# Kernel optimization log

Measured on AMD Instinct MI355X. Metric: run time of the kernel, lower is better.

The kernel has to match this reference:

```python
import math
import jax, jax.numpy as jnp
import numpy as np

B, L, HID = 2, 2048, 2048
H = 16
D = HID // H  # 128
EPS = 1e-6
ROPE_BASE = 10000.0
BETA_MIN, BETA_MAX = 0.8, 0.9995


def _rope_cache(seq_len, dim):
    half = dim // 2
    inv_freq = 1.0 / (ROPE_BASE ** (jnp.arange(half, dtype=jnp.float32) / float(half)))
    t = jnp.arange(seq_len, dtype=jnp.float32)
    freqs = t[:, None] * inv_freq[None, :]  # [L, half]
    return jnp.cos(freqs), jnp.sin(freqs)


def _apply_rope(x, cos, sin):
    # x: [B, H, L, D]; cos/sin: [L, D//2]
    half = x.shape[-1] // 2
    xe, xo = x[..., :half], x[..., half:]
    c = cos[None, None]
    s = sin[None, None]
    return jnp.concatenate([xe * c - xo * s, xe * s + xo * c], axis=-1)


def setup_inputs() -> dict:
    key = jax.random.key(0)
    ks = jax.random.split(key, 6)
    sc = 1.0 / math.sqrt(HID)  # ~ xavier scale
    return {
        "x": jax.random.normal(ks[0], (B, L, HID), jnp.float32),
        "Wq": jax.random.normal(ks[1], (HID, HID), jnp.float32) * sc,
        "Wk": jax.random.normal(ks[2], (HID, HID), jnp.float32) * sc,
        "Wv": jax.random.normal(ks[3], (HID, HID), jnp.float32) * sc,
        "Wg": jax.random.normal(ks[4], (HID, H), jnp.float32) * sc,
        "bg": jnp.full((H,), math.log(0.98 / (1.0 - 0.98)), jnp.float32),
        "Wo": jax.random.normal(ks[5], (HID, HID), jnp.float32) * sc,
        "bo": jnp.zeros((HID,), jnp.float32),
    }


def _deltanet(x, Wq, Wk, Wv, Wg, bg, Wo, bo):
    Bb, Ll, _ = x.shape
    split = lambda t: t.reshape(Bb, Ll, H, D).transpose(0, 2, 1, 3)  # [B,H,L,D]
    q = split(x @ Wq)
    k = split(x @ Wk)
    v = split(x @ Wv)

    cos, sin = _rope_cache(Ll, D)
    q = _apply_rope(q, cos, sin)
    k = _apply_rope(k, cos, sin)

    beta = jax.nn.sigmoid(x @ Wg + bg)                # [B,L,H]
    beta = jnp.clip(beta, BETA_MIN, BETA_MAX).transpose(0, 2, 1)  # [B,H,L]

    phi_q = jax.nn.elu(q) + 1.0
    phi_k = jax.nn.elu(k) + 1.0

    # time-major for scan
    pq = phi_q.transpose(2, 0, 1, 3)  # [L,B,H,D]
    pk = phi_k.transpose(2, 0, 1, 3)
    vt = v.transpose(2, 0, 1, 3)
    bt = beta.transpose(2, 0, 1)      # [L,B,H]

    S0 = jnp.zeros((Bb, H, D, D), jnp.float32)
    z0 = jnp.zeros((Bb, H, D), jnp.float32)

    def step(carry, inp):
        S, z = carry
        pq_t, pk_t, v_t, b_t = inp
        S = S * b_t[..., None, None] + pk_t[..., :, None] * v_t[..., None, :]
        z = z * b_t[..., None] + pk_t
        numer = jnp.einsum('bhd,bhde->bhe', pq_t, S)
        denom = jnp.sum(pq_t * z, axis=-1, keepdims=True) + EPS
        return (S, z), numer / denom

    (_, _), y = jax.lax.scan(step, (S0, z0), (pq, pk, vt, bt))  # y: [L,B,H,D]
    y = y.transpose(1, 0, 2, 3).reshape(Bb, Ll, HID)  # [B,L,H*D]
    return y @ Wo + bo


def reference(x, Wq, Wk, Wv, Wg, bg, Wo, bo):
    return _deltanet(x, Wq, Wk, Wv, Wg, bg, Wo, bo)
```

## Files before the change

kernel.cpp:

```cpp
#include <hip/hip_runtime.h>


typedef __attribute__((ext_vector_type(8))) short short8;
typedef __attribute__((ext_vector_type(4))) float f32x4;

__device__ __forceinline__ unsigned short f2bf(float f) {
  unsigned u = __float_as_uint(f);
  u += 0x7fffu + ((u >> 16) & 1u);
  return (unsigned short)(u >> 16);
}
__device__ __forceinline__ float bf2f(unsigned short s) {
  return __uint_as_float(((unsigned)s) << 16);
}
__device__ __forceinline__ float phi_elu1(float x) {
  return x > 0.f ? x + 1.f : expf(x);
}
__device__ __forceinline__ void gl_lds16(const void* g, void* l) {
  __builtin_amdgcn_global_load_lds(
      (const __attribute__((address_space(1))) void*)g,
      (__attribute__((address_space(3))) void*)l, 16, 0, 0);
}
__device__ __forceinline__ void bar_raw() {
  asm volatile("" ::: "memory");
  __builtin_amdgcn_s_barrier();
  asm volatile("" ::: "memory");
}

__global__ __launch_bounds__(256)
void k_cast(const float* __restrict__ x, unsigned short* __restrict__ xb) {
  int i = (blockIdx.x * 256 + threadIdx.x) * 4;
  float4 f = *(const float4*)(x + i);
  uint2 p;
  p.x = (unsigned)f2bf(f.x) | ((unsigned)f2bf(f.y) << 16);
  p.y = (unsigned)f2bf(f.z) | ((unsigned)f2bf(f.w) << 16);
  *(uint2*)(xb + i) = p;
}

__global__ __launch_bounds__(256)
void k_transw(const float* __restrict__ Wq, const float* __restrict__ Wk,
              const float* __restrict__ Wv, const float* __restrict__ Wo,
              const float* __restrict__ Wg,
              unsigned short* __restrict__ Wt, unsigned short* __restrict__ Wot,
              unsigned short* __restrict__ Wgt16) {
  const int z = blockIdx.z;
  if (z == 4) {
    if (blockIdx.y != 0) return;
    int idx = blockIdx.x * 256 + threadIdx.x;
    int h = idx >> 9, k4 = (idx & 511) * 4;
    uint2 p;
    p.x = (unsigned)f2bf(Wg[(k4 + 0) * 16 + h]) | ((unsigned)f2bf(Wg[(k4 + 1) * 16 + h]) << 16);
    p.y = (unsigned)f2bf(Wg[(k4 + 2) * 16 + h]) | ((unsigned)f2bf(Wg[(k4 + 3) * 16 + h]) << 16);
    *(uint2*)(Wgt16 + (size_t)h * 2048 + k4) = p;
    return;
  }
  const float* W = (z == 0) ? Wq : (z == 1) ? Wk : (z == 2) ? Wv : Wo;
  unsigned short* out = (z < 3) ? (Wt + (size_t)z * 2048 * 2048) : Wot;
  __shared__ float tile[64][65];
  const int n0 = blockIdx.x * 64;
  const int k0 = blockIdx.y * 64;
  const int tx = threadIdx.x & 63;
  const int ty = threadIdx.x >> 6;
#pragma unroll
  for (int rl = 0; rl < 16; ++rl) {
    int kk = rl * 4 + ty;
    tile[kk][tx] = W[(size_t)(k0 + kk) * 2048 + n0 + tx];
  }
  __syncthreads();
#pragma unroll
  for (int rl = 0; rl < 16; ++rl) {
    int nn = rl * 4 + ty;
    out[(size_t)(n0 + nn) * 2048 + k0 + tx] = f2bf(tile[tx][nn]);
  }
}

__global__ __launch_bounds__(256)
void k_betaW(const unsigned short* __restrict__ xb, const unsigned short* __restrict__ Wgt16,
             const float* __restrict__ bg, float* __restrict__ beta) {
  const int w = threadIdx.x >> 6;
  const int lane = threadIdx.x & 63;
  const int m = blockIdx.x * 4 + w;
  const int h = lane & 15, kq = lane >> 4;
  const unsigned short* xr = xb + (size_t)m * 2048 + kq * 512;
  const unsigned short* wr = Wgt16 + (size_t)h * 2048 + kq * 512;
  float acc = 0.f;
#pragma unroll 8
  for (int i = 0; i < 64; ++i) {
    short8 xv = *(const short8*)(xr + i * 8);
    short8 wv = *(const short8*)(wr + i * 8);
#pragma unroll
    for (int j = 0; j < 8; ++j)
      acc = fmaf(bf2f((unsigned short)xv[j]), bf2f((unsigned short)wv[j]), acc);
  }
  acc += __shfl_xor(acc, 16, 64);
  acc += __shfl_xor(acc, 32, 64);
  if (lane < 16) {
    float v = acc + bg[h];
    float bv = 1.f / (1.f + expf(-v));
    beta[(size_t)m * 16 + h] = fminf(fmaxf(bv, 0.8f), 0.9995f);
  }
}

template <bool OUT_BF16, bool ADD_BIAS>
__global__ __launch_bounds__(256)
void k_gemm(const unsigned short* __restrict__ A, const unsigned short* __restrict__ Bt,
            void* __restrict__ Cptr, const float* __restrict__ bias,
            int M, int N, int K, int ldA, int ldC) {
  __shared__ __align__(16) unsigned short As[128][64];
  __shared__ __align__(16) unsigned short Bs[128][64];
  const int tid = threadIdx.x;
  const int n0 = blockIdx.x * 128;
  const int m0 = blockIdx.y * 128;
  const int lane = tid & 63;
  const int w = tid >> 6;
  const int wm = w >> 1, wn = w & 1;
  const int q = lane >> 4, r = lane & 15;

  const int srow0 = w * 8 + (lane >> 3);
  const int scol = ((lane & 7) ^ ((lane >> 3) & 7)) * 8;

  f32x4 acc[4][4];
#pragma unroll
  for (int i = 0; i < 4; ++i)
#pragma unroll
    for (int j = 0; j < 4; ++j) acc[i][j] = (f32x4){0.f, 0.f, 0.f, 0.f};

  const unsigned short* A0 = A + (size_t)(m0 + srow0) * ldA + scol;
  const unsigned short* B0 = Bt + (size_t)(n0 + srow0) * K + scol;
  unsigned short* lA = &As[srow0][(lane & 7) * 8];
  unsigned short* lB = &Bs[srow0][(lane & 7) * 8];

  const int rsw = r & 7;

  for (int kt = 0; kt < K; kt += 64) {
    __syncthreads();
#pragma unroll
    for (int i = 0; i < 4; ++i) {
      gl_lds16(A0 + (size_t)i * 32 * ldA + kt, lA + i * 2048);
      gl_lds16(B0 + (size_t)i * 32 * K + kt, lB + i * 2048);
    }
    __syncthreads();
#pragma unroll
    for (int kk = 0; kk < 2; ++kk) {
      const int ps = ((kk * 4 + q) ^ rsw) * 8;
      short8 af[4], bfr[4];
#pragma unroll
      for (int i = 0; i < 4; ++i)
        af[i] = *(const short8*)&As[wm * 64 + i * 16 + r][ps];
#pragma unroll
      for (int j = 0; j < 4; ++j)
        bfr[j] = *(const short8*)&Bs[wn * 64 + j * 16 + r][ps];
#pragma unroll
      for (int i = 0; i < 4; ++i)
#pragma unroll
        for (int j = 0; j < 4; ++j)
          acc[i][j] = __builtin_amdgcn_mfma_f32_16x16x32_bf16(af[i], bfr[j], acc[i][j], 0, 0, 0);
    }
  }
#pragma unroll
  for (int i = 0; i < 4; ++i) {
#pragma unroll
    for (int j = 0; j < 4; ++j) {
#pragma unroll
      for (int rr = 0; rr < 4; ++rr) {
        int mi = m0 + wm * 64 + i * 16 + q * 4 + rr;
        int ni = n0 + wn * 64 + j * 16 + r;
        float val = acc[i][j][rr];
        if (ADD_BIAS) val += bias[ni];
        if (OUT_BF16)
          ((unsigned short*)Cptr)[(size_t)mi * ldC + ni] = f2bf(val);
        else
          ((float*)Cptr)[(size_t)mi * ldC + ni] = val;
      }
    }
  }
}

template <bool OUT_BF16, bool ADD_BIAS>
__global__ __launch_bounds__(512, 2)
void k_gemm2(const unsigned short* __restrict__ A, const unsigned short* __restrict__ Bt,
             void* __restrict__ Cptr, const float* __restrict__ bias,
             int M, int N, int K, int ldA, int ldC) {
  __shared__ __align__(16) unsigned short Ls[3][3][128][64];
  const int tid = threadIdx.x;
  const int lane = tid & 63;
  const int w = tid >> 6;
  const int wm = w >> 1;
  const int wn = w & 1;
  const int ql = lane >> 4;
  const int r = lane & 15;

  const int nwg = gridDim.x * gridDim.y;
  const int orig = blockIdx.y * gridDim.x + blockIdx.x;
  const int li = (orig & 7) * (nwg >> 3) + (orig >> 3);
  const int m0 = (li & 15) * 256;
  const int n0 = (li >> 4) * 128;

  const int srow = tid >> 3;
  const int sphys = tid & 7;
  const int slog = sphys ^ (srow & 7);
  const unsigned short* Ab = A + (size_t)(m0 + srow) * ldA + slog * 8;
  const unsigned short* Bb = Bt + (size_t)(n0 + srow) * K + slog * 8;

#define STG(st, h, tt)                                                        \
  do {                                                                        \
    const size_t ldx = ((h) == 2) ? (size_t)K : (size_t)ldA;                  \
    const unsigned short* gs =                                                \
        (((h) == 2) ? Bb : (Ab + (size_t)((h) * 128) * ldA)) +                \
        (size_t)(tt) * 64;                                                    \
    unsigned short* ld = &Ls[(st)][(h)][srow][sphys * 8];                     \
    gl_lds16(gs, ld);                                                         \
    gl_lds16(gs + 64 * ldx, ld + 64 * 64);                                    \
  } while (0)

  f32x4 acc[4][4];
#pragma unroll
  for (int i = 0; i < 4; ++i)
#pragma unroll
    for (int j = 0; j < 4; ++j) acc[i][j] = (f32x4){0.f, 0.f, 0.f, 0.f};

  const int NT = K >> 6;

#pragma unroll
  for (int h = 0; h < 3; ++h) STG(0, h, 0);
#pragma unroll
  for (int h = 0; h < 3; ++h) STG(1, h, 1);
  asm volatile("s_waitcnt vmcnt(6)" ::: "memory");
  bar_raw();

  short8 bfr[4][2];

  for (int t = 0; t < NT; ++t) {
    const int st = t % 3;
    const unsigned short (*LA)[64] = Ls[st][wm >> 1];
    const unsigned short (*LB)[64] = Ls[st][2];
    const int arow0 = (wm & 1) * 64;
    const int brow0 = wn * 64;
    const bool pf = (t + 2 < NT);
    const int s2 = (t + 2) % 3;
#pragma unroll
    for (int p = 0; p < 2; ++p) {
      if (p == 0) {
#pragma unroll
        for (int nj = 0; nj < 4; ++nj)
#pragma unroll
          for (int kk = 0; kk < 2; ++kk)
            bfr[nj][kk] = *(const short8*)
                &LB[brow0 + nj * 16 + r][((kk * 4 + ql) ^ (r & 7)) * 8];
      }
      short8 af[2][2];
#pragma unroll
      for (int im = 0; im < 2; ++im)
#pragma unroll
        for (int kk = 0; kk < 2; ++kk)
          af[im][kk] = *(const short8*)
              &LA[arow0 + (p * 2 + im) * 16 + r][((kk * 4 + ql) ^ (r & 7)) * 8];
      if (pf) {
        if (p == 0) {
          STG(s2, 0, t + 2);
          STG(s2, 1, t + 2);
        } else {
          STG(s2, 2, t + 2);
        }
      }
      bar_raw();
      __builtin_amdgcn_s_setprio(1);
#pragma unroll
      for (int kk = 0; kk < 2; ++kk)
#pragma unroll
        for (int im = 0; im < 2; ++im)
#pragma unroll
          for (int nj = 0; nj < 4; ++nj)
            acc[p * 2 + im][nj] = __builtin_amdgcn_mfma_f32_16x16x32_bf16(
                af[im][kk], bfr[nj][kk], acc[p * 2 + im][nj], 0, 0, 0);
      __builtin_amdgcn_s_setprio(0);
      if (p == 1) {
        if (pf)
          asm volatile("s_waitcnt vmcnt(6)" ::: "memory");
        else if (t + 1 < NT)
          asm volatile("s_waitcnt vmcnt(0)" ::: "memory");
      }
      __builtin_amdgcn_sched_barrier(0);
      bar_raw();
    }
  }
#undef STG

#pragma unroll
  for (int mi = 0; mi < 4; ++mi) {
#pragma unroll
    for (int nj = 0; nj < 4; ++nj) {
#pragma unroll
      for (int rr = 0; rr < 4; ++rr) {
        int mrow = m0 + wm * 64 + mi * 16 + ql * 4 + rr;
        int ncol = n0 + wn * 64 + nj * 16 + r;
        float val = acc[mi][nj][rr];
        if (ADD_BIAS) val += bias[ncol];
        if (OUT_BF16)
          ((unsigned short*)Cptr)[(size_t)mrow * ldC + ncol] = f2bf(val);
        else
          ((float*)Cptr)[(size_t)mrow * ldC + ncol] = val;
      }
    }
  }
}

__global__ __launch_bounds__(256)
void k_prep(const unsigned short* __restrict__ qkv, const float* __restrict__ beta,
            unsigned short* __restrict__ Qt, unsigned short* __restrict__ Ktg,
            unsigned short* __restrict__ Ag, float* __restrict__ gch) {
  const int ch = blockIdx.x;
  const int bh = blockIdx.y;
  const int b = bh >> 4, h = bh & 15;
  const int tid = threadIdx.x;
  const int t0 = ch * 64;

  __shared__ float Gs[64];
  __shared__ unsigned short Qs[64][136];
  __shared__ unsigned short Ks[64][136];

  if (tid < 64) {
    float bb = beta[((size_t)(b * 2048 + t0 + tid)) * 16 + h];
#pragma unroll
    for (int off = 1; off < 64; off <<= 1) {
      float o = __shfl_up(bb, off, 64);
      if (tid >= off) bb *= o;
    }
    Gs[tid] = bb;
    if (tid == 63) gch[bh * 32 + ch] = bb;
  }
  __syncthreads();

  const int dgl = tid & 7;
  float invf[8];
#pragma unroll
  for (int j = 0; j < 8; ++j)
    invf[j] = expf((float)(dgl * 8 + j) * -0.14391156831212787f);

  int s = tid >> 3;
#pragma unroll
  for (int rep = 0; rep < 2; ++rep, s += 32) {
    size_t row = ((size_t)(b * 2048 + t0 + s)) * 6144 + (size_t)h * 128;
    short8 qlo = *(const short8*)(qkv + row + dgl * 8);
    short8 qhi = *(const short8*)(qkv + row + 64 + dgl * 8);
    short8 klo = *(const short8*)(qkv + row + 2048 + dgl * 8);
    short8 khi = *(const short8*)(qkv + row + 2048 + 64 + dgl * 8);
    float g = Gs[s];
    float ig = 1.f / g;
    float tg = (float)(t0 + s);
    short8 oql, oqh, okl, okh;
#pragma unroll
    for (int j = 0; j < 8; ++j) {
      float sn, cs;
      __sincosf(tg * invf[j], &sn, &cs);
      float qe = bf2f((unsigned short)qlo[j]), qo = bf2f((unsigned short)qhi[j]);
      float a0 = qe * cs - qo * sn, a1 = qe * sn + qo * cs;
      oql[j] = (short)f2bf(phi_elu1(a0) * g);
      oqh[j] = (short)f2bf(phi_elu1(a1) * g);
      float ke = bf2f((unsigned short)klo[j]), ko = bf2f((unsigned short)khi[j]);
      a0 = ke * cs - ko * sn;
      a1 = ke * sn + ko * cs;
      okl[j] = (short)f2bf(phi_elu1(a0) * ig);
      okh[j] = (short)f2bf(phi_elu1(a1) * ig);
    }
    size_t qbase = (((size_t)bh * 32 + ch) * 64 + s) * 128;
    *(short8*)(Qt + qbase + dgl * 8) = oql;
    *(short8*)(Qt + qbase + 64 + dgl * 8) = oqh;
    *(short8*)&Qs[s][dgl * 8] = oql;
    *(short8*)&Qs[s][64 + dgl * 8] = oqh;
    *(short8*)&Ks[s][dgl * 8] = okl;
    *(short8*)&Ks[s][64 + dgl * 8] = okh;
  }
  __syncthreads();

  {
    const int d = tid >> 1, sh = tid & 1;
    unsigned pk[16];
#pragma unroll
    for (int i = 0; i < 16; ++i)
      pk[i] = (unsigned)Ks[sh * 32 + 2 * i][d] | ((unsigned)Ks[sh * 32 + 2 * i + 1][d] << 16);
    unsigned short* kr = Ktg + ((size_t)bh * 32 + ch) * 8192 + (size_t)d * 64 + sh * 32;
#pragma unroll
    for (int i = 0; i < 4; ++i)
      *(uint4*)(kr + i * 8) = *(uint4*)&pk[i * 4];
  }

  {
    const int lane = tid & 63;
    const int w = tid >> 6;
    const int q = lane >> 4, r = lane & 15;
    f32x4 acc[4];
#pragma unroll
    for (int nt = 0; nt < 4; ++nt) acc[nt] = (f32x4){0.f, 0.f, 0.f, 0.f};
#pragma unroll
    for (int kk = 0; kk < 4; ++kk) {
      short8 af = *(const short8*)&Qs[w * 16 + r][kk * 32 + q * 8];
#pragma unroll
      for (int nt = 0; nt < 4; ++nt) {
        short8 bf = *(const short8*)&Ks[nt * 16 + r][kk * 32 + q * 8];
        acc[nt] = __builtin_amdgcn_mfma_f32_16x16x32_bf16(af, bf, acc[nt], 0, 0, 0);
      }
    }
    unsigned short* Agp = Ag + ((size_t)bh * 32 + ch) * 4096;
#pragma unroll
    for (int nt = 0; nt < 4; ++nt) {
#pragma unroll
      for (int rr = 0; rr < 4; ++rr) {
        int t_l = w * 16 + q * 4 + rr;
        int s_l = nt * 16 + r;
        float val = (s_l <= t_l) ? acc[nt][rr] : 0.f;
        Agp[t_l * 64 + s_l] = f2bf(val);
      }
    }
  }
}

__global__ __launch_bounds__(512)
void k_scan(const unsigned short* __restrict__ Qt, const unsigned short* __restrict__ Ktg,
            const unsigned short* __restrict__ Ag, const unsigned short* __restrict__ qkv,
            const float* __restrict__ gch, unsigned short* __restrict__ numerb) {
  const int bh = blockIdx.x;
  const int b = bh >> 4, h = bh & 15;
  const int tid = threadIdx.x;
  const int lane = tid & 63;
  const int w = tid >> 6;
  const int q = lane >> 4, r = lane & 15;

  __shared__ unsigned short Qs[64][136];
  __shared__ unsigned short Kts[128][72];
  __shared__ unsigned short As[64][72];
  __shared__ unsigned short Vt[128][72];
  __shared__ unsigned short SbT[8][16][136];
  __shared__ __align__(16) float zbuf[2][128];
  __shared__ float invs[64];

  f32x4 S_acc[8];
#pragma unroll
  for (int i = 0; i < 8; ++i) S_acc[i] = (f32x4){0.f, 0.f, 0.f, 0.f};
  if (tid < 128) zbuf[0][tid] = 0.f;

  for (int ch = 0; ch < 32; ++ch) {
    const int cur = ch & 1, nxt = cur ^ 1;
    __syncthreads();
    {
      const unsigned short* Qg = Qt + ((size_t)bh * 32 + ch) * 8192;
#pragma unroll
      for (int i = 0; i < 2; ++i) {
        int c = tid + i * 512;
        int ss = c >> 4, dg = c & 15;
        *(int4*)&Qs[ss][dg * 8] = *(const int4*)(Qg + ss * 128 + dg * 8);
      }
      const unsigned short* Kg = Ktg + ((size_t)bh * 32 + ch) * 8192;
#pragma unroll
      for (int i = 0; i < 2; ++i) {
        int c = tid + i * 512;
        int d = c >> 3, sg = c & 7;
        *(int4*)&Kts[d][sg * 8] = *(const int4*)(Kg + d * 64 + sg * 8);
      }
      const unsigned short* Agp = Ag + ((size_t)bh * 32 + ch) * 4096;
      {
        int t_l = tid >> 3, sg = tid & 7;
        *(int4*)&As[t_l][sg * 8] = *(const int4*)(Agp + t_l * 64 + sg * 8);
      }
      {
        int ss = tid >> 3, ef = tid & 7;
        const unsigned short* vrow =
            qkv + ((size_t)(b * 2048 + ch * 64 + ss)) * 6144 + 4096 + h * 128;
#pragma unroll
        for (int rep = 0; rep < 4; ++rep) {
          int e4 = ef + rep * 8;
          uint2 vv = *(const uint2*)(vrow + e4 * 4);
          const unsigned short* pv = (const unsigned short*)&vv;
#pragma unroll
          for (int j = 0; j < 4; ++j) Vt[e4 * 4 + j][ss] = pv[j];
        }
      }
#pragma unroll
      for (int ib = 0; ib < 8; ++ib) {
        uint2 pk;
        pk.x = (unsigned)f2bf(S_acc[ib][0]) | ((unsigned)f2bf(S_acc[ib][1]) << 16);
        pk.y = (unsigned)f2bf(S_acc[ib][2]) | ((unsigned)f2bf(S_acc[ib][3]) << 16);
        *(uint2*)&SbT[w][r][ib * 16 + q * 4] = pk;
      }
    }
    __syncthreads();

    const float gc = gch[bh * 32 + ch];

    f32x4 nacc[4];
#pragma unroll
    for (int wb = 0; wb < 4; ++wb) nacc[wb] = (f32x4){0.f, 0.f, 0.f, 0.f};
#pragma unroll
    for (int kk = 0; kk < 4; ++kk) {
      short8 sb = *(const short8*)&SbT[w][r][kk * 32 + q * 8];
#pragma unroll
      for (int wb = 0; wb < 4; ++wb) {
        short8 aq = *(const short8*)&Qs[wb * 16 + r][kk * 32 + q * 8];
        nacc[wb] = __builtin_amdgcn_mfma_f32_16x16x32_bf16(aq, sb, nacc[wb], 0, 0, 0);
      }
    }
    short8 vf[2];
#pragma unroll
    for (int kk = 0; kk < 2; ++kk) {
      vf[kk] = *(const short8*)&Vt[w * 16 + r][kk * 32 + q * 8];
#pragma unroll
      for (int wb = 0; wb < 4; ++wb) {
        short8 aa = *(const short8*)&As[wb * 16 + r][kk * 32 + q * 8];
        nacc[wb] = __builtin_amdgcn_mfma_f32_16x16x32_bf16(aa, vf[kk], nacc[wb], 0, 0, 0);
      }
    }

    if (w < 4) {
      float dsum = 0.f;
#pragma unroll
      for (int kk = 0; kk < 4; ++kk) {
        short8 aq = *(const short8*)&Qs[w * 16 + r][kk * 32 + q * 8];
        const float* zp = &zbuf[cur][kk * 32 + q * 8];
        float4 z0a = *(const float4*)zp;
        float4 z0b = *(const float4*)(zp + 4);
        dsum = fmaf(bf2f((unsigned short)aq[0]), z0a.x, dsum);
        dsum = fmaf(bf2f((unsigned short)aq[1]), z0a.y, dsum);
        dsum = fmaf(bf2f((unsigned short)aq[2]), z0a.z, dsum);
        dsum = fmaf(bf2f((unsigned short)aq[3]), z0a.w, dsum);
        dsum = fmaf(bf2f((unsigned short)aq[4]), z0b.x, dsum);
        dsum = fmaf(bf2f((unsigned short)aq[5]), z0b.y, dsum);
        dsum = fmaf(bf2f((unsigned short)aq[6]), z0b.z, dsum);
        dsum = fmaf(bf2f((unsigned short)aq[7]), z0b.w, dsum);
      }
#pragma unroll
      for (int kk = 0; kk < 2; ++kk) {
        short8 aa = *(const short8*)&As[w * 16 + r][kk * 32 + q * 8];
#pragma unroll
        for (int j = 0; j < 8; ++j) dsum += bf2f((unsigned short)aa[j]);
      }
      dsum += __shfl_xor(dsum, 16, 64);
      dsum += __shfl_xor(dsum, 32, 64);
      if (lane < 16) invs[w * 16 + lane] = 1.f / (dsum + 1e-6f);
    }

    {
      int d = tid >> 2, qt = tid & 3;
      const unsigned short* kp = &Kts[d][qt * 16];
      float zs = 0.f;
#pragma unroll
      for (int i = 0; i < 2; ++i) {
        short8 kv = *(const short8*)(kp + i * 8);
#pragma unroll
        for (int j = 0; j < 8; ++j) zs += bf2f((unsigned short)kv[j]);
      }
      zs += __shfl_xor(zs, 1, 64);
      zs += __shfl_xor(zs, 2, 64);
      if (qt == 0) zbuf[nxt][d] = gc * (zbuf[cur][d] + zs);
    }

#pragma unroll
    for (int ib = 0; ib < 8; ++ib) {
#pragma unroll
      for (int kk = 0; kk < 2; ++kk) {
        short8 ak = *(const short8*)&Kts[ib * 16 + r][kk * 32 + q * 8];
        S_acc[ib] = __builtin_amdgcn_mfma_f32_16x16x32_bf16(ak, vf[kk], S_acc[ib], 0, 0, 0);
      }
#pragma unroll
      for (int rr = 0; rr < 4; ++rr) S_acc[ib][rr] *= gc;
    }

    __syncthreads();

#pragma unroll
    for (int wb = 0; wb < 4; ++wb) {
#pragma unroll
      for (int rr = 0; rr < 4; ++rr) {
        int t_l = wb * 16 + q * 4 + rr;
        float inv_r = invs[t_l];
        size_t m = (size_t)b * 2048 + ch * 64 + t_l;
        numerb[m * 2048 + h * 128 + w * 16 + r] = f2bf(nacc[wb][rr] * inv_r);
      }
    }
  }
}

extern "C" void kernel_launch(void* const* d_in, const int* in_sizes, int n_in,
                              void* d_out, int out_size, void* d_ws, size_t ws_size,
                              hipStream_t stream) {
  const float* x  = (const float*)d_in[0];
  const float* Wq = (const float*)d_in[1];
  const float* Wk = (const float*)d_in[2];
  const float* Wv = (const float*)d_in[3];
  const float* Wg = (const float*)d_in[4];
  const float* bg = (const float*)d_in[5];
  const float* Wo = (const float*)d_in[6];
  const float* bo = (const float*)d_in[7];

  char* ws = (char*)d_ws;
  unsigned short* xb    = (unsigned short*)(ws);
  unsigned short* Qt    = (unsigned short*)(ws);
  unsigned short* Wt    = (unsigned short*)(ws + 16777216);
  unsigned short* Ktg   = (unsigned short*)(ws + 16777216);
  unsigned short* Ag    = (unsigned short*)(ws + 33554432);
  unsigned short* Wot   = (unsigned short*)(ws + 41943040);
  unsigned short* qkvb  = (unsigned short*)(ws + 50331648);
  float*          beta  = (float*)(ws + 100663296);
  unsigned short* Wgt16 = (unsigned short*)(ws + 101187584);
  unsigned short* numerb= (unsigned short*)(ws + 101187584);
  float*          gch   = (float*)d_out;

  k_cast<<<8192, 256, 0, stream>>>(x, xb);
  k_transw<<<dim3(32, 32, 5), 256, 0, stream>>>(Wq, Wk, Wv, Wo, Wg, Wt, Wot, Wgt16);
  k_gemm<true, false><<<dim3(48, 32), 256, 0, stream>>>(
      xb, Wt, qkvb, nullptr, 4096, 6144, 2048, 2048, 6144);
  k_betaW<<<1024, 256, 0, stream>>>(xb, Wgt16, bg, beta);
  k_prep<<<dim3(32, 32), 256, 0, stream>>>(qkvb, beta, Qt, Ktg, Ag, gch);
  k_scan<<<32, 512, 0, stream>>>(Qt, Ktg, Ag, qkvb, gch, numerb);
  k_gemm2<false, true><<<dim3(16, 16), 512, 0, stream>>>(
      numerb, Wot, d_out, bo, 4096, 2048, 2048, 2048, 2048);
}
```

Measured before the change: 469.8 us.

## Split sequential chunk scan into parallel per-chunk KV, prefix scan, and output kernels

The old k_scan ran only 32 blocks, one per batch-head, walking 32 chunks in sequence and keeping the state in registers, which left most of the GPU idle. The new code computes each chunk's K^T V and key sums in parallel (k_kv), runs a light decayed prefix scan over chunk states in global memory (k_sprefix), then computes chunk outputs in parallel (k_out). It also writes transposed V from k_prep and moves workspace buffers around. The cost is extra global traffic for the per-chunk state matrices, stored in bf16, plus two more kernel launches.

```diff
diff --git a/kernel.cpp b/kernel.cpp
--- a/kernel.cpp
+++ b/kernel.cpp
@@ -307,7 +307,8 @@
 __global__ __launch_bounds__(256)
 void k_prep(const unsigned short* __restrict__ qkv, const float* __restrict__ beta,
             unsigned short* __restrict__ Qt, unsigned short* __restrict__ Ktg,
-            unsigned short* __restrict__ Ag, float* __restrict__ gch) {
+            unsigned short* __restrict__ Ag, unsigned short* __restrict__ Vg,
+            float* __restrict__ gch) {
   const int ch = blockIdx.x;
   const int bh = blockIdx.y;
   const int b = bh >> 4, h = bh & 15;
@@ -317,6 +318,7 @@
   __shared__ float Gs[64];
   __shared__ unsigned short Qs[64][136];
   __shared__ unsigned short Ks[64][136];
+  __shared__ unsigned short Vs[128][72];
 
   if (tid < 64) {
     float bb = beta[((size_t)(b * 2048 + t0 + tid)) * 16 + h];
@@ -370,6 +372,17 @@
     *(short8*)&Ks[s][dgl * 8] = okl;
     *(short8*)&Ks[s][64 + dgl * 8] = okh;
   }
+  {
+    const int s2 = tid >> 2, qe = tid & 3;
+    const unsigned short* vrow =
+        qkv + ((size_t)(b * 2048 + t0 + s2)) * 6144 + 4096 + (size_t)h * 128 + qe * 32;
+#pragma unroll
+    for (int i = 0; i < 4; ++i) {
+      short8 vv = *(const short8*)(vrow + i * 8);
+#pragma unroll
+      for (int j = 0; j < 8; ++j) Vs[qe * 32 + i * 8 + j][s2] = (unsigned short)vv[j];
+    }
+  }
   __syncthreads();
 
   {
@@ -382,6 +395,10 @@
 #pragma unroll
     for (int i = 0; i < 4; ++i)
       *(uint4*)(kr + i * 8) = *(uint4*)&pk[i * 4];
+    unsigned short* vr = Vg + ((size_t)bh * 32 + ch) * 8192 + (size_t)d * 64 + sh * 32;
+#pragma unroll
+    for (int i = 0; i < 4; ++i)
+      *(uint4*)(vr + i * 8) = *(const uint4*)&Vs[d][sh * 32 + i * 8];
   }
 
   {
@@ -414,166 +431,210 @@
   }
 }
 
-__global__ __launch_bounds__(512)
-void k_scan(const unsigned short* __restrict__ Qt, const unsigned short* __restrict__ Ktg,
-            const unsigned short* __restrict__ Ag, const unsigned short* __restrict__ qkv,
-            const float* __restrict__ gch, unsigned short* __restrict__ numerb) {
-  const int bh = blockIdx.x;
+__global__ __launch_bounds__(256)
+void k_kv(const unsigned short* __restrict__ Ktg, const unsigned short* __restrict__ Vg,
+          unsigned short* __restrict__ Mg, float* __restrict__ mzg) {
+  const int ch = blockIdx.x, bh = blockIdx.y;
+  const int tid = threadIdx.x, lane = tid & 63, w = tid >> 6;
+  const int q = lane >> 4, r = lane & 15;
+  __shared__ unsigned short Kts[128][72];
+  __shared__ unsigned short Vs[128][72];
+  const unsigned short* Kp = Ktg + ((size_t)bh * 32 + ch) * 8192;
+  const unsigned short* Vp = Vg + ((size_t)bh * 32 + ch) * 8192;
+#pragma unroll
+  for (int i = 0; i < 4; ++i) {
+    int c = tid + i * 256;
+    int dd = c >> 3, sg = c & 7;
+    *(int4*)&Kts[dd][sg * 8] = *(const int4*)(Kp + dd * 64 + sg * 8);
+    *(int4*)&Vs[dd][sg * 8] = *(const int4*)(Vp + dd * 64 + sg * 8);
+  }
+  __syncthreads();
+  f32x4 acc[2][8];
+#pragma unroll
+  for (int jj = 0; jj < 2; ++jj)
+#pragma unroll
+    for (int i = 0; i < 8; ++i) acc[jj][i] = (f32x4){0.f, 0.f, 0.f, 0.f};
+#pragma unroll
+  for (int kk = 0; kk < 2; ++kk) {
+    short8 af[2];
+    af[0] = *(const short8*)&Vs[(w * 2 + 0) * 16 + r][kk * 32 + q * 8];
+    af[1] = *(const short8*)&Vs[(w * 2 + 1) * 16 + r][kk * 32 + q * 8];
+#pragma unroll
+    for (int i = 0; i < 8; ++i) {
+      short8 bf = *(const short8*)&Kts[i * 16 + r][kk * 32 + q * 8];
+      acc[0][i] = __builtin_amdgcn_mfma_f32_16x16x32_bf16(af[0], bf, acc[0][i], 0, 0, 0);
+      acc[1][i] = __builtin_amdgcn_mfma_f32_16x16x32_bf16(af[1], bf, acc[1][i], 0, 0, 0);
+    }
+  }
+  {
+    int dd = tid >> 1, sh = tid & 1;
+    const unsigned short* kp = &Kts[dd][sh * 32];
+    float zs = 0.f;
+#pragma unroll
+    for (int i = 0; i < 4; ++i) {
+      short8 kv = *(const short8*)(kp + i * 8);
+#pragma unroll
+      for (int j = 0; j < 8; ++j) zs += bf2f((unsigned short)kv[j]);
+    }
+    zs += __shfl_xor(zs, 1, 64);
+    if (sh == 0) mzg[((size_t)bh * 32 + ch) * 128 + dd] = zs;
+  }
+  unsigned short* Mp = Mg + ((size_t)bh * 32 + ch) * 16384;
+#pragma unroll
+  for (int jj = 0; jj < 2; ++jj)
+#pragma unroll
+    for (int i = 0; i < 8; ++i)
+#pragma unroll
+      for (int rr = 0; rr < 4; ++rr) {
+        int e = (w * 2 + jj) * 16 + q * 4 + rr;
+        Mp[e * 128 + i * 16 + r] = f2bf(acc[jj][i][rr]);
+      }
+}
+
+__global__ __launch_bounds__(256)
+void k_sprefix(unsigned short* __restrict__ Msg, float* __restrict__ mzg,
+               const float* __restrict__ gch) {
+  const int es = blockIdx.x;
+  const int bh = blockIdx.y;
+  const int tid = threadIdx.x;
+  const int e = es * 16 + (tid >> 4);
+  const int d0 = (tid & 15) * 8;
+  unsigned short* base = Msg + (size_t)bh * 32 * 16384 + (size_t)e * 128 + d0;
+  const float* gp = gch + bh * 32;
+  float sv[8];
+#pragma unroll
+  for (int i = 0; i < 8; ++i) sv[i] = 0.f;
+  uint4 mcur = *(const uint4*)base;
+  for (int c = 0; c < 32; ++c) {
+    uint4 mnext;
+    if (c < 31) mnext = *(const uint4*)(base + (size_t)(c + 1) * 16384);
+    uint4 so;
+    so.x = (unsigned)f2bf(sv[0]) | ((unsigned)f2bf(sv[1]) << 16);
+    so.y = (unsigned)f2bf(sv[2]) | ((unsigned)f2bf(sv[3]) << 16);
+    so.z = (unsigned)f2bf(sv[4]) | ((unsigned)f2bf(sv[5]) << 16);
+    so.w = (unsigned)f2bf(sv[6]) | ((unsigned)f2bf(sv[7]) << 16);
+    *(uint4*)(base + (size_t)c * 16384) = so;
+    float g = gp[c];
+    const unsigned short* mp = (const unsigned short*)&mcur;
+#pragma unroll
+    for (int i = 0; i < 8; ++i) sv[i] = g * (sv[i] + bf2f(mp[i]));
+    mcur = mnext;
+  }
+  if (es == 0 && tid < 128) {
+    float* zb = mzg + (size_t)bh * 32 * 128 + tid;
+    float z = 0.f;
+    float zc = zb[0];
+    for (int c = 0; c < 32; ++c) {
+      float znext = (c < 31) ? zb[(size_t)(c + 1) * 128] : 0.f;
+      zb[(size_t)c * 128] = z;
+      z = gp[c] * (z + zc);
+      zc = znext;
+    }
+  }
+}
+
+__global__ __launch_bounds__(256)
+void k_out(const unsigned short* __restrict__ Qt, const unsigned short* __restrict__ Sg,
+           const unsigned short* __restrict__ Ag, const unsigned short* __restrict__ Vg,
+           const float* __restrict__ zg, unsigned short* __restrict__ numerb) {
+  const int ch = blockIdx.x, bh = blockIdx.y;
   const int b = bh >> 4, h = bh & 15;
-  const int tid = threadIdx.x;
-  const int lane = tid & 63;
-  const int w = tid >> 6;
+  const int tid = threadIdx.x, lane = tid & 63, w = tid >> 6;
   const int q = lane >> 4, r = lane & 15;
-
   __shared__ unsigned short Qs[64][136];
-  __shared__ unsigned short Kts[128][72];
+  __shared__ unsigned short Ss[128][136];
   __shared__ unsigned short As[64][72];
-  __shared__ unsigned short Vt[128][72];
-  __shared__ unsigned short SbT[8][16][136];
-  __shared__ __align__(16) float zbuf[2][128];
+  __shared__ unsigned short Vs[128][72];
+  __shared__ float zc[128];
   __shared__ float invs[64];
 
-  f32x4 S_acc[8];
-#pragma unroll
-  for (int i = 0; i < 8; ++i) S_acc[i] = (f32x4){0.f, 0.f, 0.f, 0.f};
-  if (tid < 128) zbuf[0][tid] = 0.f;
-
-  for (int ch = 0; ch < 32; ++ch) {
-    const int cur = ch & 1, nxt = cur ^ 1;
-    __syncthreads();
-    {
-      const unsigned short* Qg = Qt + ((size_t)bh * 32 + ch) * 8192;
-#pragma unroll
-      for (int i = 0; i < 2; ++i) {
-        int c = tid + i * 512;
-        int ss = c >> 4, dg = c & 15;
-        *(int4*)&Qs[ss][dg * 8] = *(const int4*)(Qg + ss * 128 + dg * 8);
-      }
-      const unsigned short* Kg = Ktg + ((size_t)bh * 32 + ch) * 8192;
-#pragma unroll
-      for (int i = 0; i < 2; ++i) {
-        int c = tid + i * 512;
-        int d = c >> 3, sg = c & 7;
-        *(int4*)&Kts[d][sg * 8] = *(const int4*)(Kg + d * 64 + sg * 8);
-      }
-      const unsigned short* Agp = Ag + ((size_t)bh * 32 + ch) * 4096;
-      {
-        int t_l = tid >> 3, sg = tid & 7;
-        *(int4*)&As[t_l][sg * 8] = *(const int4*)(Agp + t_l * 64 + sg * 8);
-      }
-      {
-        int ss = tid >> 3, ef = tid & 7;
-        const unsigned short* vrow =
-            qkv + ((size_t)(b * 2048 + ch * 64 + ss)) * 6144 + 4096 + h * 128;
-#pragma unroll
-        for (int rep = 0; rep < 4; ++rep) {
-          int e4 = ef + rep * 8;
-          uint2 vv = *(const uint2*)(vrow + e4 * 4);
-          const unsigned short* pv = (const unsigned short*)&vv;
-#pragma unroll
-          for (int j = 0; j < 4; ++j) Vt[e4 * 4 + j][ss] = pv[j];
-        }
-      }
-#pragma unroll
-      for (int ib = 0; ib < 8; ++ib) {
-        uint2 pk;
-        pk.x = (unsigned)f2bf(S_acc[ib][0]) | ((unsigned)f2bf(S_acc[ib][1]) << 16);
-        pk.y = (unsigned)f2bf(S_acc[ib][2]) | ((unsigned)f2bf(S_acc[ib][3]) << 16);
-        *(uint2*)&SbT[w][r][ib * 16 + q * 4] = pk;
-      }
-    }
-    __syncthreads();
-
-    const float gc = gch[bh * 32 + ch];
-
-    f32x4 nacc[4];
-#pragma unroll
-    for (int wb = 0; wb < 4; ++wb) nacc[wb] = (f32x4){0.f, 0.f, 0.f, 0.f};
+  const unsigned short* Qg = Qt + ((size_t)bh * 32 + ch) * 8192;
+#pragma unroll
+  for (int i = 0; i < 4; ++i) {
+    int c = tid + i * 256;
+    int ss = c >> 4, dg = c & 15;
+    *(int4*)&Qs[ss][dg * 8] = *(const int4*)(Qg + ss * 128 + dg * 8);
+  }
+  const unsigned short* Sp = Sg + ((size_t)bh * 32 + ch) * 16384;
+#pragma unroll
+  for (int i = 0; i < 8; ++i) {
+    int c = tid + i * 256;
+    int e = c >> 4, dg = c & 15;
+    *(int4*)&Ss[e][dg * 8] = *(const int4*)(Sp + e * 128 + dg * 8);
+  }
+#pragma unroll
+  for (int i = 0; i < 2; ++i) {
+    int c = tid + i * 256;
+    int t_l = c >> 3, sg = c & 7;
+    *(int4*)&As[t_l][sg * 8] =
+        *(const int4*)(Ag + ((size_t)bh * 32 + ch) * 4096 + t_l * 64 + sg * 8);
+  }
+  const unsigned short* Vp = Vg + ((size_t)bh * 32 + ch) * 8192;
+#pragma unroll
+  for (int i = 0; i < 4; ++i) {
+    int c = tid + i * 256;
+    int e = c >> 3, sg = c & 7;
+    *(int4*)&Vs[e][sg * 8] = *(const int4*)(Vp + e * 64 + sg * 8);
+  }
+  if (tid < 128) zc[tid] = zg[((size_t)bh * 32 + ch) * 128 + tid];
+  __syncthreads();
+
+  f32x4 nacc[8];
+#pragma unroll
+  for (int j = 0; j < 8; ++j) nacc[j] = (f32x4){0.f, 0.f, 0.f, 0.f};
+#pragma unroll
+  for (int kk = 0; kk < 4; ++kk) {
+    short8 aq = *(const short8*)&Qs[w * 16 + r][kk * 32 + q * 8];
+#pragma unroll
+    for (int j = 0; j < 8; ++j) {
+      short8 bf = *(const short8*)&Ss[j * 16 + r][kk * 32 + q * 8];
+      nacc[j] = __builtin_amdgcn_mfma_f32_16x16x32_bf16(aq, bf, nacc[j], 0, 0, 0);
+    }
+  }
+#pragma unroll
+  for (int kk = 0; kk < 2; ++kk) {
+    short8 aa = *(const short8*)&As[w * 16 + r][kk * 32 + q * 8];
+#pragma unroll
+    for (int j = 0; j < 8; ++j) {
+      short8 bf = *(const short8*)&Vs[j * 16 + r][kk * 32 + q * 8];
+      nacc[j] = __builtin_amdgcn_mfma_f32_16x16x32_bf16(aa, bf, nacc[j], 0, 0, 0);
+    }
+  }
+  {
+    float dsum = 0.f;
 #pragma unroll
     for (int kk = 0; kk < 4; ++kk) {
-      short8 sb = *(const short8*)&SbT[w][r][kk * 32 + q * 8];
-#pragma unroll
-      for (int wb = 0; wb < 4; ++wb) {
-        short8 aq = *(const short8*)&Qs[wb * 16 + r][kk * 32 + q * 8];
-        nacc[wb] = __builtin_amdgcn_mfma_f32_16x16x32_bf16(aq, sb, nacc[wb], 0, 0, 0);
-      }
-    }
-    short8 vf[2];
+      short8 aq = *(const short8*)&Qs[w * 16 + r][kk * 32 + q * 8];
+      const float* zp = &zc[kk * 32 + q * 8];
+      float4 z0a = *(const float4*)zp;
+      float4 z0b = *(const float4*)(zp + 4);
+      dsum = fmaf(bf2f((unsigned short)aq[0]), z0a.x, dsum);
+      dsum = fmaf(bf2f((unsigned short)aq[1]), z0a.y, dsum);
+      dsum = fmaf(bf2f((unsigned short)aq[2]), z0a.z, dsum);
+      dsum = fmaf(bf2f((unsigned short)aq[3]), z0a.w, dsum);
+      dsum = fmaf(bf2f((unsigned short)aq[4]), z0b.x, dsum);
+      dsum = fmaf(bf2f((unsigned short)aq[5]), z0b.y, dsum);
+      dsum = fmaf(bf2f((unsigned short)aq[6]), z0b.z, dsum);
+      dsum = fmaf(bf2f((unsigned short)aq[7]), z0b.w, dsum);
+    }
 #pragma unroll
     for (int kk = 0; kk < 2; ++kk) {
-      vf[kk] = *(const short8*)&Vt[w * 16 + r][kk * 32 + q * 8];
-#pragma unroll
-      for (int wb = 0; wb < 4; ++wb) {
-        short8 aa = *(const short8*)&As[wb * 16 + r][kk * 32 + q * 8];
-        nacc[wb] = __builtin_amdgcn_mfma_f32_16x16x32_bf16(aa, vf[kk], nacc[wb], 0, 0, 0);
-      }
-    }
-
-    if (w < 4) {
-      float dsum = 0.f;
-#pragma unroll
-      for (int kk = 0; kk < 4; ++kk) {
-        short8 aq = *(const short8*)&Qs[w * 16 + r][kk * 32 + q * 8];
-        const float* zp = &zbuf[cur][kk * 32 + q * 8];
-        float4 z0a = *(const float4*)zp;
-        float4 z0b = *(const float4*)(zp + 4);
-        dsum = fmaf(bf2f((unsigned short)aq[0]), z0a.x, dsum);
-        dsum = fmaf(bf2f((unsigned short)aq[1]), z0a.y, dsum);
-        dsum = fmaf(bf2f((unsigned short)aq[2]), z0a.z, dsum);
-        dsum = fmaf(bf2f((unsigned short)aq[3]), z0a.w, dsum);
-        dsum = fmaf(bf2f((unsigned short)aq[4]), z0b.x, dsum);
-        dsum = fmaf(bf2f((unsigned short)aq[5]), z0b.y, dsum);
-        dsum = fmaf(bf2f((unsigned short)aq[6]), z0b.z, dsum);
-        dsum = fmaf(bf2f((unsigned short)aq[7]), z0b.w, dsum);
-      }
-#pragma unroll
-      for (int kk = 0; kk < 2; ++kk) {
-        short8 aa = *(const short8*)&As[w * 16 + r][kk * 32 + q * 8];
-#pragma unroll
-        for (int j = 0; j < 8; ++j) dsum += bf2f((unsigned short)aa[j]);
-      }
-      dsum += __shfl_xor(dsum, 16, 64);
-      dsum += __shfl_xor(dsum, 32, 64);
-      if (lane < 16) invs[w * 16 + lane] = 1.f / (dsum + 1e-6f);
-    }
-
-    {
-      int d = tid >> 2, qt = tid & 3;
-      const unsigned short* kp = &Kts[d][qt * 16];
-      float zs = 0.f;
-#pragma unroll
-      for (int i = 0; i < 2; ++i) {
-        short8 kv = *(const short8*)(kp + i * 8);
-#pragma unroll
-        for (int j = 0; j < 8; ++j) zs += bf2f((unsigned short)kv[j]);
-      }
-      zs += __shfl_xor(zs, 1, 64);
-      zs += __shfl_xor(zs, 2, 64);
-      if (qt == 0) zbuf[nxt][d] = gc * (zbuf[cur][d] + zs);
-    }
-
-#pragma unroll
-    for (int ib = 0; ib < 8; ++ib) {
-#pragma unroll
-      for (int kk = 0; kk < 2; ++kk) {
-        short8 ak = *(const short8*)&Kts[ib * 16 + r][kk * 32 + q * 8];
-        S_acc[ib] = __builtin_amdgcn_mfma_f32_16x16x32_bf16(ak, vf[kk], S_acc[ib], 0, 0, 0);
-      }
-#pragma unroll
-      for (int rr = 0; rr < 4; ++rr) S_acc[ib][rr] *= gc;
-    }
-
-    __syncthreads();
-
-#pragma unroll
-    for (int wb = 0; wb < 4; ++wb) {
-#pragma unroll
-      for (int rr = 0; rr < 4; ++rr) {
-        int t_l = wb * 16 + q * 4 + rr;
-        float inv_r = invs[t_l];
-        size_t m = (size_t)b * 2048 + ch * 64 + t_l;
-        numerb[m * 2048 + h * 128 + w * 16 + r] = f2bf(nacc[wb][rr] * inv_r);
-      }
+      short8 aa = *(const short8*)&As[w * 16 + r][kk * 32 + q * 8];
+#pragma unroll
+      for (int j = 0; j < 8; ++j) dsum += bf2f((unsigned short)aa[j]);
+    }
+    dsum += __shfl_xor(dsum, 16, 64);
+    dsum += __shfl_xor(dsum, 32, 64);
+    if (lane < 16) invs[w * 16 + lane] = 1.f / (dsum + 1e-6f);
+  }
+  __syncthreads();
+#pragma unroll
+  for (int j = 0; j < 8; ++j) {
+#pragma unroll
+    for (int rr = 0; rr < 4; ++rr) {
+      int t_l = w * 16 + q * 4 + rr;
+      size_t m = (size_t)b * 2048 + ch * 64 + t_l;
+      numerb[m * 2048 + h * 128 + j * 16 + r] = f2bf(nacc[j][rr] * invs[t_l]);
     }
   }
 }
@@ -598,9 +659,12 @@
   unsigned short* Ag    = (unsigned short*)(ws + 33554432);
   unsigned short* Wot   = (unsigned short*)(ws + 41943040);
   unsigned short* qkvb  = (unsigned short*)(ws + 50331648);
-  float*          beta  = (float*)(ws + 100663296);
-  unsigned short* Wgt16 = (unsigned short*)(ws + 101187584);
-  unsigned short* numerb= (unsigned short*)(ws + 101187584);
+  unsigned short* Mg    = (unsigned short*)(ws + 50331648);
+  float*          mzg   = (float*)(ws + 83886080);
+  unsigned short* numerb= (unsigned short*)(ws + 100663296);
+  unsigned short* Vg    = (unsigned short*)(ws + 117440512);
+  float*          beta  = (float*)(ws + 134217728);
+  unsigned short* Wgt16 = (unsigned short*)(ws + 134479872);
   float*          gch   = (float*)d_out;
 
   k_cast<<<8192, 256, 0, stream>>>(x, xb);
@@ -608,8 +672,10 @@
   k_gemm<true, false><<<dim3(48, 32), 256, 0, stream>>>(
       xb, Wt, qkvb, nullptr, 4096, 6144, 2048, 2048, 6144);
   k_betaW<<<1024, 256, 0, stream>>>(xb, Wgt16, bg, beta);
-  k_prep<<<dim3(32, 32), 256, 0, stream>>>(qkvb, beta, Qt, Ktg, Ag, gch);
-  k_scan<<<32, 512, 0, stream>>>(Qt, Ktg, Ag, qkvb, gch, numerb);
+  k_prep<<<dim3(32, 32), 256, 0, stream>>>(qkvb, beta, Qt, Ktg, Ag, Vg, gch);
+  k_kv<<<dim3(32, 32), 256, 0, stream>>>(Ktg, Vg, Mg, mzg);
+  k_sprefix<<<dim3(8, 32), 256, 0, stream>>>(Mg, mzg, gch);
+  k_out<<<dim3(32, 32), 256, 0, stream>>>(Qt, Mg, Ag, Vg, mzg, numerb);
   k_gemm2<false, true><<<dim3(16, 16), 512, 0, stream>>>(
       numerb, Wot, d_out, bo, 4096, 2048, 2048, 2048, 2048);
 }
```

Measured after the change: 407.0 us. 1.15x faster.
